# Kernel optimization log

Measured on AMD Instinct MI355X. Metric: run time of the kernel, lower is better.

The kernel has to match this reference:

```python
import jax, jax.numpy as jnp
import numpy as np

B, T, C, P = 512, 365, 10, 64  # batch, num_steps, input_dim, num_prototypes


def setup_inputs() -> dict:
    key = jax.random.key(0)
    k1, k2, k3, k4 = jax.random.split(key, 4)
    input_seq = jax.random.normal(k1, (B, T, C), dtype=jnp.float32)
    # binary observation mask (some dates missing)
    mask = (jax.random.uniform(k2, (B, T)) > 0.1).astype(jnp.float32)
    label = jax.random.randint(k3, (B,), 0, P)
    prototypes = jax.random.normal(k4, (P, T, C), dtype=jnp.float32)
    return {"input_seq": input_seq, "mask": mask, "label": label,
            "prototypes": prototypes}


def reference(input_seq, mask, label, prototypes):
    # distances[b,p] = sum_{t,c} mask[b,t] * (x[b,t,c] - proto[p,t,c])^2
    # expanded so we never materialize the [B,P,T,C] broadcast:
    #   = sum mask*x^2  - 2*sum mask*x*p + sum mask*p^2
    x2 = jnp.einsum('btc,btc,bt->b', input_seq, input_seq, mask)          # [B]
    xp = jnp.einsum('btc,bt,ptc->bp', input_seq, mask, prototypes)        # [B,P]
    p2 = jnp.einsum('bt,ptc,ptc->bp', mask, prototypes, prototypes)       # [B,P]
    distances = x2[:, None] - 2.0 * xp + p2                               # [B,P]
    indices = jnp.argmin(distances, axis=1)                               # [B]
    # gather selected prototype per sample (trans/offset inactive -> shared protos)
    output_seq = prototypes[indices]                                      # [B,T,C]
    return (output_seq, input_seq, distances, indices, label, mask)
```

## Files before the change

kernel.cpp:

```cpp
#include <hip/hip_runtime.h>

#define B_   512
#define T_   365
#define C_   10
#define P_   64
#define K_   3650
#define K2_  1825
#define KP2_ 1856
#define TP_  372

#define OFF_OUT0 0u
#define OFF_IN   1868800u
#define OFF_DIST 3737600u
#define OFF_IDX  3770368u
#define OFF_LAB  3770880u
#define OFF_MASK 3771392u

__global__ __launch_bounds__(1024, 4) void dist_kernel(
    const float* __restrict__ x, const float* __restrict__ mask,
    const float* __restrict__ protos, float* __restrict__ out)
{
    __shared__ float xm[4][2 * KP2_];
    __shared__ float mrow[4][TP_];

    const int tid  = threadIdx.x;
    const int lane = tid & 63;
    const int wv   = tid >> 6;
    const int h    = blockIdx.x & 1;
    const int g    = blockIdx.x >> 1;
    const int b0   = g * 4;

    for (int j = tid; j < 4 * TP_; j += 1024) {
        const int r = j / TP_;
        const int t = j - r * TP_;
        float m = 0.f;
        if (t < T_) {
            m = mask[(size_t)(b0 + r) * T_ + t];
            if (h == 0) out[OFF_MASK + (size_t)(b0 + r) * T_ + t] = m;
        }
        mrow[r][t] = m;
    }
    __syncthreads();

#pragma unroll
    for (int r = 0; r < 4; ++r) {
        const float2* xr = (const float2*)(x + (size_t)(b0 + r) * K_);
        float2*       er = (float2*)(out + OFF_IN + (size_t)(b0 + r) * K_);
        float2*       sx = (float2*)&xm[r][0];
        for (int i2 = tid; i2 < KP2_; i2 += 1024) {
            float2 v = {0.f, 0.f};
            if (i2 < K2_) {
                v = xr[i2];
                if (h == 0) er[i2] = v;
                const unsigned t = (unsigned)i2 / 5u;
                const float m = mrow[r][t];
                v.x *= m;
                v.y *= m;
            }
            sx[i2] = v;
        }
    }
    __syncthreads();

    const int pidx = h * 32 + wv * 2;
    const float2* pr0 = (const float2*)(protos + (size_t)pidx * K_);
    const float2* pr1 = (const float2*)(protos + (size_t)(pidx + 1) * K_);

    float2 a0[4], a1[4];
    float  c0[4], c1[4];
#pragma unroll
    for (int r = 0; r < 4; ++r) {
        a0[r] = {0.f, 0.f}; a1[r] = {0.f, 0.f};
        c0[r] = 0.f; c1[r] = 0.f;
    }

#pragma unroll 4
    for (int it = 0; it < 29; ++it) {
        const int i2  = it * 64 + lane;
        const int i2c = i2 < K2_ ? i2 : (K2_ - 1);
        const unsigned t = (unsigned)i2 / 5u;
        const float2 pv0 = pr0[i2c];
        const float2 pv1 = pr1[i2c];
        const float s0 = fmaf(pv0.x, pv0.x, pv0.y * pv0.y);
        const float s1 = fmaf(pv1.x, pv1.x, pv1.y * pv1.y);
#pragma unroll
        for (int r = 0; r < 4; ++r) {
            const float2 u = ((const float2*)&xm[r][0])[i2];
            const float  m = mrow[r][t];
            a0[r].x = fmaf(u.x, pv0.x, a0[r].x);
            a0[r].y = fmaf(u.y, pv0.y, a0[r].y);
            a1[r].x = fmaf(u.x, pv1.x, a1[r].x);
            a1[r].y = fmaf(u.y, pv1.y, a1[r].y);
            c0[r] = fmaf(m, s0, c0[r]);
            c1[r] = fmaf(m, s1, c1[r]);
        }
    }

#pragma unroll
    for (int r = 0; r < 4; ++r) {
        float v0 = fmaf(-2.f, a0[r].x + a0[r].y, c0[r]);
        float v1 = fmaf(-2.f, a1[r].x + a1[r].y, c1[r]);
        for (int off = 32; off; off >>= 1) {
            v0 += __shfl_down(v0, off);
            v1 += __shfl_down(v1, off);
        }
        if (lane == 0) {
            out[OFF_DIST + (size_t)(b0 + r) * P_ + pidx]     = v0;
            out[OFF_DIST + (size_t)(b0 + r) * P_ + pidx + 1] = v1;
        }
    }
}

__global__ __launch_bounds__(256) void argmin_kernel(
    const float* __restrict__ x, const float* __restrict__ mask,
    const int* __restrict__ label, const float* __restrict__ protos,
    float* __restrict__ out)
{
    __shared__ float red[4];
    __shared__ float x2sh;
    __shared__ int   sel;

    const int b    = blockIdx.x;
    const int tid  = threadIdx.x;
    const int lane = tid & 63;
    const int wv   = tid >> 6;

    const float2* xr = (const float2*)(x + (size_t)b * K_);
    const float*  mr = mask + (size_t)b * T_;
    float s = 0.f;
    for (int i2 = tid; i2 < K2_; i2 += 256) {
        const float2 v = xr[i2];
        const float  m = mr[(unsigned)i2 / 5u];
        s = fmaf(m, fmaf(v.x, v.x, v.y * v.y), s);
    }
    for (int off = 32; off; off >>= 1) s += __shfl_down(s, off);
    if (lane == 0) red[wv] = s;
    __syncthreads();
    if (tid == 0) x2sh = red[0] + red[1] + red[2] + red[3];
    __syncthreads();

    if (tid < 64) {
        const float x2 = x2sh;
        float v = out[OFF_DIST + (size_t)b * P_ + tid] + x2;
        out[OFF_DIST + (size_t)b * P_ + tid] = v;
        int idx = tid;
        for (int off = 32; off; off >>= 1) {
            float ov = __shfl_down(v, off);
            int   oi = __shfl_down(idx, off);
            if (ov < v || (ov == v && oi < idx)) { v = ov; idx = oi; }
        }
        if (tid == 0) {
            sel = idx;
            out[OFF_IDX + b] = (float)idx;
            out[OFF_LAB + b] = (float)label[b];
        }
    }
    __syncthreads();

    const float2* src = (const float2*)(protos + (size_t)sel * K_);
    float2* dst = (float2*)(out + OFF_OUT0 + (size_t)b * K_);
    for (int i2 = tid; i2 < K2_; i2 += 256) dst[i2] = src[i2];
}

extern "C" void kernel_launch(void* const* d_in, const int* in_sizes, int n_in,
                              void* d_out, int out_size, void* d_ws, size_t ws_size,
                              hipStream_t stream) {
    const float* x      = (const float*)d_in[0];
    const float* mask   = (const float*)d_in[1];
    const int*   label  = (const int*)d_in[2];
    const float* protos = (const float*)d_in[3];
    float* out = (float*)d_out;

    dist_kernel<<<256, 1024, 0, stream>>>(x, mask, protos, out);
    argmin_kernel<<<B_, 256, 0, stream>>>(x, mask, label, protos, out);
}
```

Baseline: 91.73 us.

## Precompute per-timestep prototype norms and split distance work across more blocks

```diff
diff --git a/kernel.cpp b/kernel.cpp
--- a/kernel.cpp
+++ b/kernel.cpp
@@ -6,8 +6,7 @@
 #define P_   64
 #define K_   3650
 #define K2_  1825
-#define KP2_ 1856
-#define TP_  372
+#define XROW 3712
 
 #define OFF_OUT0 0u
 #define OFF_IN   1868800u
@@ -16,140 +15,174 @@
 #define OFF_LAB  3770880u
 #define OFF_MASK 3771392u
 
-__global__ __launch_bounds__(1024, 4) void dist_kernel(
+#define WS_X2 0
+#define WS_SP 512
+
+__global__ __launch_bounds__(512, 4) void dist_kernel(
     const float* __restrict__ x, const float* __restrict__ mask,
-    const float* __restrict__ protos, float* __restrict__ out)
+    const float* __restrict__ protos, float* __restrict__ out,
+    float* __restrict__ ws)
 {
-    __shared__ float xm[4][2 * KP2_];
-    __shared__ float mrow[4][TP_];
+    __shared__ float xm[4][XROW];
+    __shared__ float mrow[4][368];
+    __shared__ float r2[8][4];
 
     const int tid  = threadIdx.x;
     const int lane = tid & 63;
     const int wv   = tid >> 6;
-    const int h    = blockIdx.x & 1;
-    const int g    = blockIdx.x >> 1;
+    const int g    = blockIdx.x >> 2;
+    const int q    = blockIdx.x & 3;
     const int b0   = g * 4;
 
-    for (int j = tid; j < 4 * TP_; j += 1024) {
-        const int r = j / TP_;
-        const int t = j - r * TP_;
+    if (tid < 46) {
+        int j = blockIdx.x * 46 + tid;
+        if (j < T_ * P_) {
+            int t = j >> 6, p = j & 63;
+            const float* pp = protos + (size_t)p * K_ + t * C_;
+            float s = 0.f;
+#pragma unroll
+            for (int c = 0; c < C_; ++c) s = fmaf(pp[c], pp[c], s);
+            ws[WS_SP + j] = s;
+        }
+    }
+
+    for (int j = tid; j < 4 * 368; j += 512) {
+        const int r = j >> 9 ? 0 : 0;  (void)r;
+        const int rr = j / 368;
+        const int t  = j - rr * 368;
         float m = 0.f;
         if (t < T_) {
-            m = mask[(size_t)(b0 + r) * T_ + t];
-            if (h == 0) out[OFF_MASK + (size_t)(b0 + r) * T_ + t] = m;
-        }
-        mrow[r][t] = m;
-    }
-    __syncthreads();
-
+            m = mask[(size_t)(b0 + rr) * T_ + t];
+            if (q == 0) out[OFF_MASK + (size_t)(b0 + rr) * T_ + t] = m;
+        }
+        mrow[rr][t] = m;
+    }
+    __syncthreads();
+
+    float s2[4] = {0.f, 0.f, 0.f, 0.f};
 #pragma unroll
     for (int r = 0; r < 4; ++r) {
         const float2* xr = (const float2*)(x + (size_t)(b0 + r) * K_);
-        float2*       er = (float2*)(out + OFF_IN + (size_t)(b0 + r) * K_);
+        float*        eb = out + OFF_IN + (size_t)(b0 + r) * K_;
         float2*       sx = (float2*)&xm[r][0];
-        for (int i2 = tid; i2 < KP2_; i2 += 1024) {
-            float2 v = {0.f, 0.f};
-            if (i2 < K2_) {
-                v = xr[i2];
-                if (h == 0) er[i2] = v;
-                const unsigned t = (unsigned)i2 / 5u;
-                const float m = mrow[r][t];
-                v.x *= m;
-                v.y *= m;
+        for (int i2 = tid; i2 < K2_; i2 += 512) {
+            float2 v = xr[i2];
+            if (q == 0) {
+                __builtin_nontemporal_store(v.x, eb + 2 * i2);
+                __builtin_nontemporal_store(v.y, eb + 2 * i2 + 1);
             }
+            const float m = mrow[r][(unsigned)i2 / 5u];
+            v.x *= m; v.y *= m;
             sx[i2] = v;
-        }
-    }
-    __syncthreads();
-
-    const int pidx = h * 32 + wv * 2;
+            s2[r] = fmaf(v.x, v.x, fmaf(v.y, v.y, s2[r]));
+        }
+    }
+#pragma unroll
+    for (int r = 0; r < 4; ++r) {
+        float v = s2[r];
+        for (int off = 32; off; off >>= 1) v += __shfl_down(v, off);
+        if (lane == 0) r2[wv][r] = v;
+    }
+    __syncthreads();
+    if (q == 0 && tid < 4) {
+        float s = 0.f;
+#pragma unroll
+        for (int w = 0; w < 8; ++w) s += r2[w][tid];
+        ws[WS_X2 + b0 + tid] = s;
+    }
+
+    const int pidx = q * 16 + wv * 2;
     const float2* pr0 = (const float2*)(protos + (size_t)pidx * K_);
     const float2* pr1 = (const float2*)(protos + (size_t)(pidx + 1) * K_);
 
     float2 a0[4], a1[4];
-    float  c0[4], c1[4];
+#pragma unroll
+    for (int r = 0; r < 4; ++r) { a0[r] = {0.f, 0.f}; a1[r] = {0.f, 0.f}; }
+
+#pragma unroll 2
+    for (int it = 0; it < 14; ++it) {
+        const int i4 = it * 64 + lane;
+        const float2 p0l = pr0[2 * i4], p0h = pr0[2 * i4 + 1];
+        const float2 p1l = pr1[2 * i4], p1h = pr1[2 * i4 + 1];
+#pragma unroll
+        for (int r = 0; r < 4; ++r) {
+            const float4 u = ((const float4*)&xm[r][0])[i4];
+            a0[r].x = fmaf(u.x, p0l.x, a0[r].x);
+            a0[r].y = fmaf(u.y, p0l.y, a0[r].y);
+            a0[r].x = fmaf(u.z, p0h.x, a0[r].x);
+            a0[r].y = fmaf(u.w, p0h.y, a0[r].y);
+            a1[r].x = fmaf(u.x, p1l.x, a1[r].x);
+            a1[r].y = fmaf(u.y, p1l.y, a1[r].y);
+            a1[r].x = fmaf(u.z, p1h.x, a1[r].x);
+            a1[r].y = fmaf(u.w, p1h.y, a1[r].y);
+        }
+    }
+    {
+        const int i2 = 1792 + lane;
+        if (i2 < K2_) {
+            const float2 pv0 = pr0[i2];
+            const float2 pv1 = pr1[i2];
+#pragma unroll
+            for (int r = 0; r < 4; ++r) {
+                const float2 u = ((const float2*)&xm[r][0])[i2];
+                a0[r].x = fmaf(u.x, pv0.x, a0[r].x);
+                a0[r].y = fmaf(u.y, pv0.y, a0[r].y);
+                a1[r].x = fmaf(u.x, pv1.x, a1[r].x);
+                a1[r].y = fmaf(u.y, pv1.y, a1[r].y);
+            }
+        }
+    }
+
 #pragma unroll
     for (int r = 0; r < 4; ++r) {
-        a0[r] = {0.f, 0.f}; a1[r] = {0.f, 0.f};
-        c0[r] = 0.f; c1[r] = 0.f;
-    }
-
-#pragma unroll 4
-    for (int it = 0; it < 29; ++it) {
-        const int i2  = it * 64 + lane;
-        const int i2c = i2 < K2_ ? i2 : (K2_ - 1);
-        const unsigned t = (unsigned)i2 / 5u;
-        const float2 pv0 = pr0[i2c];
-        const float2 pv1 = pr1[i2c];
-        const float s0 = fmaf(pv0.x, pv0.x, pv0.y * pv0.y);
-        const float s1 = fmaf(pv1.x, pv1.x, pv1.y * pv1.y);
-#pragma unroll
-        for (int r = 0; r < 4; ++r) {
-            const float2 u = ((const float2*)&xm[r][0])[i2];
-            const float  m = mrow[r][t];
-            a0[r].x = fmaf(u.x, pv0.x, a0[r].x);
-            a0[r].y = fmaf(u.y, pv0.y, a0[r].y);
-            a1[r].x = fmaf(u.x, pv1.x, a1[r].x);
-            a1[r].y = fmaf(u.y, pv1.y, a1[r].y);
-            c0[r] = fmaf(m, s0, c0[r]);
-            c1[r] = fmaf(m, s1, c1[r]);
-        }
-    }
-
-#pragma unroll
-    for (int r = 0; r < 4; ++r) {
-        float v0 = fmaf(-2.f, a0[r].x + a0[r].y, c0[r]);
-        float v1 = fmaf(-2.f, a1[r].x + a1[r].y, c1[r]);
+        float v0 = a0[r].x + a0[r].y;
+        float v1 = a1[r].x + a1[r].y;
         for (int off = 32; off; off >>= 1) {
             v0 += __shfl_down(v0, off);
             v1 += __shfl_down(v1, off);
         }
         if (lane == 0) {
-            out[OFF_DIST + (size_t)(b0 + r) * P_ + pidx]     = v0;
-            out[OFF_DIST + (size_t)(b0 + r) * P_ + pidx + 1] = v1;
+            out[OFF_DIST + (size_t)(b0 + r) * P_ + pidx]     = -2.f * v0;
+            out[OFF_DIST + (size_t)(b0 + r) * P_ + pidx + 1] = -2.f * v1;
         }
     }
 }
 
 __global__ __launch_bounds__(256) void argmin_kernel(
-    const float* __restrict__ x, const float* __restrict__ mask,
-    const int* __restrict__ label, const float* __restrict__ protos,
+    const float* __restrict__ mask, const int* __restrict__ label,
+    const float* __restrict__ protos, const float* __restrict__ ws,
     float* __restrict__ out)
 {
-    __shared__ float red[4];
-    __shared__ float x2sh;
+    __shared__ float c4[4][64];
     __shared__ int   sel;
 
     const int b    = blockIdx.x;
     const int tid  = threadIdx.x;
-    const int lane = tid & 63;
-    const int wv   = tid >> 6;
-
-    const float2* xr = (const float2*)(x + (size_t)b * K_);
-    const float*  mr = mask + (size_t)b * T_;
-    float s = 0.f;
-    for (int i2 = tid; i2 < K2_; i2 += 256) {
-        const float2 v = xr[i2];
-        const float  m = mr[(unsigned)i2 / 5u];
-        s = fmaf(m, fmaf(v.x, v.x, v.y * v.y), s);
-    }
-    for (int off = 32; off; off >>= 1) s += __shfl_down(s, off);
-    if (lane == 0) red[wv] = s;
-    __syncthreads();
-    if (tid == 0) x2sh = red[0] + red[1] + red[2] + red[3];
+    const int part = tid >> 6;
+    const int p    = tid & 63;
+
+    {
+        const int t0  = part * 92;
+        const int t1  = (part == 3) ? T_ : t0 + 92;
+        const float* mb = mask + (size_t)b * T_;
+        float acc = 0.f;
+        for (int t = t0; t < t1; ++t)
+            acc = fmaf(mb[t], ws[WS_SP + t * 64 + p], acc);
+        c4[part][p] = acc;
+    }
     __syncthreads();
 
     if (tid < 64) {
-        const float x2 = x2sh;
-        float v = out[OFF_DIST + (size_t)b * P_ + tid] + x2;
-        out[OFF_DIST + (size_t)b * P_ + tid] = v;
-        int idx = tid;
+        const float c = c4[0][p] + c4[1][p] + c4[2][p] + c4[3][p];
+        float v = ws[WS_X2 + b] + c + out[OFF_DIST + (size_t)b * P_ + p];
+        out[OFF_DIST + (size_t)b * P_ + p] = v;
+        int idx = p;
         for (int off = 32; off; off >>= 1) {
             float ov = __shfl_down(v, off);
             int   oi = __shfl_down(idx, off);
             if (ov < v || (ov == v && oi < idx)) { v = ov; idx = oi; }
         }
-        if (tid == 0) {
+        if (p == 0) {
             sel = idx;
             out[OFF_IDX + b] = (float)idx;
             out[OFF_LAB + b] = (float)label[b];
@@ -158,8 +191,12 @@
     __syncthreads();
 
     const float2* src = (const float2*)(protos + (size_t)sel * K_);
-    float2* dst = (float2*)(out + OFF_OUT0 + (size_t)b * K_);
-    for (int i2 = tid; i2 < K2_; i2 += 256) dst[i2] = src[i2];
+    float* dst = out + OFF_OUT0 + (size_t)b * K_;
+    for (int i2 = tid; i2 < K2_; i2 += 256) {
+        const float2 v = src[i2];
+        __builtin_nontemporal_store(v.x, dst + 2 * i2);
+        __builtin_nontemporal_store(v.y, dst + 2 * i2 + 1);
+    }
 }
 
 extern "C" void kernel_launch(void* const* d_in, const int* in_sizes, int n_in,
@@ -170,7 +207,8 @@
     const int*   label  = (const int*)d_in[2];
     const float* protos = (const float*)d_in[3];
     float* out = (float*)d_out;
-
-    dist_kernel<<<256, 1024, 0, stream>>>(x, mask, protos, out);
-    argmin_kernel<<<B_, 256, 0, stream>>>(x, mask, label, protos, out);
+    float* ws  = (float*)d_ws;
+
+    dist_kernel<<<512, 512, 0, stream>>>(x, mask, protos, out, ws);
+    argmin_kernel<<<B_, 256, 0, stream>>>(mask, label, protos, ws, out);
 }
```

Measured after the change: 115.9 us. +26.3%, slower.
